# Kernel optimization log

Hardware: AMD Instinct MI355X
Metric: run time of the kernel (lower is better)

The kernel has to match this reference:

```python
import jax, jax.numpy as jnp
import numpy as np

INTER = 128  # in_channels // reduction

def conv1x1(x, w, b):
    # x: [B, Cin, H, W], w: [Cout, Cin], b: [Cout]
    return jnp.einsum('bchw,oc->bohw', x, w) + b[None, :, None, None]

def setup_inputs() -> dict:
    key = jax.random.key(0)
    ks = jax.random.split(key, 10)
    B, Cq, Cr, H, W = 4, 256, 512, 64, 64
    std = 0.01
    return {
        'query':     jax.random.normal(ks[0], (B, Cq, H, W), jnp.float32),
        'reference': jax.random.normal(ks[1], (B, Cr, H, W), jnp.float32),
        'Wg': jax.random.normal(ks[2], (INTER, Cr), jnp.float32) * std,
        'bg': jnp.zeros((INTER,), jnp.float32),
        'Wt': jax.random.normal(ks[3], (INTER, Cq), jnp.float32) * std,
        'bt': jnp.zeros((INTER,), jnp.float32),
        'Wp': jax.random.normal(ks[4], (INTER, Cr), jnp.float32) * std,
        'bp': jnp.zeros((INTER,), jnp.float32),
        'Wo': jax.random.normal(ks[5], (Cq, INTER), jnp.float32) * std,
        'bo': jnp.zeros((Cq,), jnp.float32),
    }

def reference(query, reference, Wg, bg, Wt, bt, Wp, bp, Wo, bo):
    B, Cq, H, W = query.shape
    HWq = H * W
    _, Cr, Hr, Wr = reference.shape
    HWr = Hr * Wr
    # 1x1-conv projections
    g_x     = conv1x1(reference, Wg, bg).reshape(B, INTER, HWr).transpose(0, 2, 1)  # [B, HWr, C']
    theta_x = conv1x1(query,     Wt, bt).reshape(B, INTER, HWq).transpose(0, 2, 1)  # [B, HWq, C']
    phi_x   = conv1x1(reference, Wp, bp).reshape(B, INTER, HWr)                     # [B, C', HWr]
    # embedded_gaussian with use_scale: scale by 1/sqrt(inter_channels)
    scores = jnp.einsum('bqc,bck->bqk', theta_x, phi_x) / jnp.sqrt(jnp.float32(INTER))
    pw = jax.nn.softmax(scores, axis=-1)                                            # [B, HWq, HWr]
    y = jnp.einsum('bqk,bkc->bqc', pw, g_x)                                          # [B, HWq, C']
    y = y.transpose(0, 2, 1).reshape(B, INTER, H, W)
    return query + conv1x1(y, Wo, bo)
```

## Files before the change

### kernel.cpp

```cpp
#include <hip/hip_runtime.h>
#include <hip/hip_bf16.h>
#include <stdint.h>

typedef short bf16x8 __attribute__((ext_vector_type(8)));
typedef float f32x4  __attribute__((ext_vector_type(4)));
typedef float f32x16 __attribute__((ext_vector_type(16)));
typedef unsigned short u16;
typedef unsigned int   u32;

#define BATCH 4
#define PTOT  4096
#define CINT  128
#define QK_SCALE 0.12751744f

__device__ __forceinline__ u32 pk_bf16(float a, float b) {
  u32 r;
  asm("v_cvt_pk_bf16_f32 %0, %1, %2" : "=v"(r) : "v"(a), "v"(b));
  return r;
}
__device__ __forceinline__ u16 f2bf(float x) { return (u16)pk_bf16(x, x); }
__device__ __forceinline__ float bf2f(u16 v) { return __uint_as_float(((u32)v) << 16); }

__device__ __forceinline__ f32x4 mfma16(bf16x8 a, bf16x8 b, f32x4 c) {
  return __builtin_amdgcn_mfma_f32_16x16x32_bf16(a, b, c, 0, 0, 0);
}
__device__ __forceinline__ f32x16 mfma32(bf16x8 a, bf16x8 b, f32x16 c) {
  return __builtin_amdgcn_mfma_f32_32x32x16_bf16(a, b, c, 0, 0, 0);
}
__device__ __forceinline__ void gload16(const u16* g, u16* l) {
  __builtin_amdgcn_global_load_lds((const __attribute__((address_space(1))) u32*)g,
                                   (__attribute__((address_space(3))) u32*)l, 16, 0, 0);
}
__device__ __forceinline__ bf16x8 mkfrag(float a0, float a1, float a2, float a3,
                                         float a4, float a5, float a6, float a7) {
  u32 A = pk_bf16(a0, a1), B = pk_bf16(a2, a3);
  u32 C = pk_bf16(a4, a5), D = pk_bf16(a6, a7);
  asm volatile("v_permlane32_swap_b32 %0, %1" : "+v"(A), "+v"(C));
  asm volatile("v_permlane32_swap_b32 %0, %1" : "+v"(B), "+v"(D));
  union { u32 w[4]; bf16x8 v; } u;
  u.w[0] = A; u.w[1] = B; u.w[2] = C; u.w[3] = D;
  return u.v;
}

__global__ void k_cvt_all(const float* __restrict__ Wt, const float* __restrict__ Wp,
                          const float* __restrict__ Wg, const float* __restrict__ Wo,
                          u16* __restrict__ dst) {
  int i = (blockIdx.x * 256 + threadIdx.x) * 4;
  const float* s; int off;
  if (i < 32768)       { s = Wt; off = i; }
  else if (i < 98304)  { s = Wp; off = i - 32768; }
  else if (i < 163840) { s = Wg; off = i - 98304; }
  else                 { s = Wo; off = i - 163840; }
  float4 v = *(const float4*)(s + off);
  *(uint2*)(dst + i) = make_uint2(pk_bf16(v.x, v.y), pk_bf16(v.z, v.w));
}

__global__ void k_proj_pix(const float* __restrict__ X, const u16* __restrict__ W,
                           const float* __restrict__ bias, u16* __restrict__ O,
                           int Cin, float scale) {
  const int b = blockIdx.y, p0 = blockIdx.x * 64;
  const int t = threadIdx.x, lane = t & 63, w = t >> 6;
  const int m_ = lane & 15, h = lane >> 4;
  __shared__ __align__(16) u16 At[64][40];
  __shared__ __align__(16) u16 Wl[128][40];
  const float* xb = X + (size_t)b * Cin * PTOT;
  f32x4 acc[4][2];
#pragma unroll
  for (int i = 0; i < 4; i++) { acc[i][0] = (f32x4)0.0f; acc[i][1] = (f32x4)0.0f; }
  const int p = t & 63, cg = t >> 6;
  const int wrow = t >> 1, whalf = t & 1;
  for (int k0 = 0; k0 < Cin; k0 += 32) {
    __syncthreads();
    {
      const float* sx = xb + (size_t)(k0 + 8 * cg) * PTOT + p0 + p;
      float v0 = sx[0],        v1 = sx[PTOT],   v2 = sx[2*PTOT], v3 = sx[3*PTOT];
      float v4 = sx[4*PTOT],   v5 = sx[5*PTOT], v6 = sx[6*PTOT], v7 = sx[7*PTOT];
      *(uint2*)&At[p][8*cg]     = make_uint2(pk_bf16(v0,v1), pk_bf16(v2,v3));
      *(uint2*)&At[p][8*cg + 4] = make_uint2(pk_bf16(v4,v5), pk_bf16(v6,v7));
    }
    {
      const u16* sw = W + (size_t)wrow * Cin + k0 + whalf * 16;
      uint4 a = *(const uint4*)sw, c = *(const uint4*)(sw + 8);
      *(uint4*)&Wl[wrow][whalf*16]     = a;
      *(uint4*)&Wl[wrow][whalf*16 + 8] = c;
    }
    __syncthreads();
    bf16x8 bf0 = *(const bf16x8*)&Wl[w*32 + m_][8*h];
    bf16x8 bf1 = *(const bf16x8*)&Wl[w*32 + 16 + m_][8*h];
#pragma unroll
    for (int mb = 0; mb < 4; mb++) {
      bf16x8 af = *(const bf16x8*)&At[mb*16 + m_][8*h];
      acc[mb][0] = mfma16(af, bf0, acc[mb][0]);
      acc[mb][1] = mfma16(af, bf1, acc[mb][1]);
    }
  }
  u16* ob = O + (size_t)b * PTOT * CINT;
#pragma unroll
  for (int mb = 0; mb < 4; mb++)
#pragma unroll
    for (int nb = 0; nb < 2; nb++) {
      int c = w*32 + nb*16 + m_;
      float bv = bias[c];
#pragma unroll
      for (int r = 0; r < 4; r++) {
        int pp = p0 + mb*16 + 4*h + r;
        ob[(size_t)pp * CINT + c] = f2bf((acc[mb][nb][r] + bv) * scale);
      }
    }
}

__global__ void k_proj_ref(const float* __restrict__ X, const u16* __restrict__ Wp,
                           const u16* __restrict__ Wg, const float* __restrict__ bp,
                           const float* __restrict__ bg, u16* __restrict__ PH,
                           u16* __restrict__ Gm) {
  const int Cin = 512;
  const int b = blockIdx.y, p0 = blockIdx.x * 64;
  const int t = threadIdx.x, lane = t & 63, w = t >> 6;
  const int m_ = lane & 15, h = lane >> 4;
  __shared__ __align__(16) u16 Bt[64][40];
  __shared__ __align__(16) u16 Wpl[128][40];
  __shared__ __align__(16) u16 Wgl[128][40];
  const float* xb = X + (size_t)b * Cin * PTOT;
  f32x4 accp[4][2];
  f32x4 accg[2][4];
#pragma unroll
  for (int i = 0; i < 4; i++) { accp[i][0] = (f32x4)0.0f; accp[i][1] = (f32x4)0.0f; }
#pragma unroll
  for (int i = 0; i < 2; i++)
#pragma unroll
    for (int j = 0; j < 4; j++) accg[i][j] = (f32x4)0.0f;
  const int p = t & 63, cg = t >> 6;
  const int wrow = t >> 1, whalf = t & 1;
  for (int k0 = 0; k0 < Cin; k0 += 32) {
    __syncthreads();
    {
      const float* sx = xb + (size_t)(k0 + 8 * cg) * PTOT + p0 + p;
      float v0 = sx[0],        v1 = sx[PTOT],   v2 = sx[2*PTOT], v3 = sx[3*PTOT];
      float v4 = sx[4*PTOT],   v5 = sx[5*PTOT], v6 = sx[6*PTOT], v7 = sx[7*PTOT];
      *(uint2*)&Bt[p][8*cg]     = make_uint2(pk_bf16(v0,v1), pk_bf16(v2,v3));
      *(uint2*)&Bt[p][8*cg + 4] = make_uint2(pk_bf16(v4,v5), pk_bf16(v6,v7));
    }
    {
      const u16* sw = Wp + (size_t)wrow * Cin + k0 + whalf * 16;
      *(uint4*)&Wpl[wrow][whalf*16]     = *(const uint4*)sw;
      *(uint4*)&Wpl[wrow][whalf*16 + 8] = *(const uint4*)(sw + 8);
      const u16* sg = Wg + (size_t)wrow * Cin + k0 + whalf * 16;
      *(uint4*)&Wgl[wrow][whalf*16]     = *(const uint4*)sg;
      *(uint4*)&Wgl[wrow][whalf*16 + 8] = *(const uint4*)(sg + 8);
    }
    __syncthreads();
    {
      bf16x8 bf0 = *(const bf16x8*)&Wpl[w*32 + m_][8*h];
      bf16x8 bf1 = *(const bf16x8*)&Wpl[w*32 + 16 + m_][8*h];
#pragma unroll
      for (int mb = 0; mb < 4; mb++) {
        bf16x8 af = *(const bf16x8*)&Bt[mb*16 + m_][8*h];
        accp[mb][0] = mfma16(af, bf0, accp[mb][0]);
        accp[mb][1] = mfma16(af, bf1, accp[mb][1]);
      }
    }
    {
      bf16x8 bfr[4];
#pragma unroll
      for (int nb = 0; nb < 4; nb++) bfr[nb] = *(const bf16x8*)&Bt[nb*16 + m_][8*h];
#pragma unroll
      for (int mb = 0; mb < 2; mb++) {
        bf16x8 af = *(const bf16x8*)&Wgl[w*32 + mb*16 + m_][8*h];
#pragma unroll
        for (int nb = 0; nb < 4; nb++) accg[mb][nb] = mfma16(af, bfr[nb], accg[mb][nb]);
      }
    }
  }
  {
    u16* ob = PH + (size_t)b * PTOT * CINT;
#pragma unroll
    for (int mb = 0; mb < 4; mb++)
#pragma unroll
      for (int nb = 0; nb < 2; nb++) {
        int c = w*32 + nb*16 + m_;
        float bv = bp[c];
#pragma unroll
        for (int r = 0; r < 4; r++) {
          int pp = p0 + mb*16 + 4*h + r;
          ob[(size_t)pp * CINT + c] = f2bf(accp[mb][nb][r] + bv);
        }
      }
  }
  {
    u16* ob = Gm + (size_t)b * CINT * PTOT;
#pragma unroll
    for (int mb = 0; mb < 2; mb++)
#pragma unroll
      for (int nb = 0; nb < 4; nb++) {
        int pidx = p0 + nb*16 + m_;
#pragma unroll
        for (int r = 0; r < 4; r++) {
          int c = w*32 + mb*16 + 4*h + r;
          ob[(size_t)c * PTOT + pidx] = f2bf(accg[mb][nb][r] + bg[c]);
        }
      }
  }
}

template<int SPLIT>
__global__ __launch_bounds__(256, 2)
void k_attn(const u16* __restrict__ TH, const u16* __restrict__ PH,
            const u16* __restrict__ G, u16* __restrict__ U,
            float* __restrict__ ML, u16* __restrict__ Y) {
  constexpr int LSPLIT = (SPLIT == 4) ? 2 : ((SPLIT == 2) ? 1 : 0);
  constexpr int NITER = 64 >> LSPLIT;
  const int total = 32 * BATCH * SPLIT;
  const int did = blockIdx.x;
  const int gid = (did & 7) * (total >> 3) + (did >> 3);
  const int qb = gid & 31, grp = gid >> 5;
  const int z = grp & (SPLIT - 1), b = grp >> LSPLIT;
  const int t = threadIdx.x, lane = t & 63, w = t >> 6;
  const int l31 = lane & 31, hi = lane >> 5;
  __shared__ __align__(16) u16 Kl[2][64 * 128];
  __shared__ __align__(16) u16 Vl[2][128 * 64];
  const u16* thb = TH + (size_t)b * PTOT * CINT;
  const u16* phb = PH + (size_t)b * PTOT * CINT;
  const u16* gb  = G  + (size_t)b * CINT * PTOT;
  const int q0 = qb * 128, qw = q0 + w * 32;
  bf16x8 qf[8];
  {
    const u16* qr = thb + (size_t)(qw + l31) * CINT + hi * 8;
#pragma unroll
    for (int cs = 0; cs < 8; cs++) qf[cs] = *(const bf16x8*)(qr + cs * 16);
  }
  f32x16 yacc[4];
#pragma unroll
  for (int i = 0; i < 4; i++) yacc[i] = (f32x16)0.0f;
  float mrun = -3.0e38f, lrun = 0.0f;
  const int it0 = z * NITER;

  auto STAGE = [&](int bb, int it) {
    const int k0 = it * 64;
#pragma unroll
    for (int i = 0; i < 4; i++) {
      const int s = w * 4 + i;
      {
        const int row = s * 4 + (lane >> 4);
        const int x = ((lane & 15) * 8) ^ ((row & 7) << 3);
        gload16(phb + (size_t)(k0 + row) * CINT + x, &Kl[bb][s * 512]);
      }
      {
        const int row = s * 8 + (lane >> 3);
        const int x = ((lane & 7) * 8) ^ ((row & 7) << 3);
        gload16(gb + (size_t)row * PTOT + k0 + x, &Vl[bb][s * 512]);
      }
    }
  };

  int cur = 0;
  STAGE(0, it0);
  for (int it = it0; it < it0 + NITER; ++it) {
    __builtin_amdgcn_s_barrier();
    if (it + 1 < it0 + NITER) {
      STAGE(cur ^ 1, it + 1);
      asm volatile("s_waitcnt vmcnt(8)" ::: "memory");
    } else {
      asm volatile("s_waitcnt vmcnt(0)" ::: "memory");
    }
    __builtin_amdgcn_s_barrier();
    __builtin_amdgcn_sched_barrier(0);
    f32x16 sa0 = (f32x16)0.0f, sa1 = (f32x16)0.0f;
    __builtin_amdgcn_s_setprio(1);
#pragma unroll
    for (int cs = 0; cs < 8; cs++) {
      const int xc = cs * 16 + hi * 8;
      const int r0 = l31, r1 = 32 + l31;
      bf16x8 a0 = *(const bf16x8*)&Kl[cur][r0 * 128 + (xc ^ ((r0 & 7) << 3))];
      bf16x8 a1 = *(const bf16x8*)&Kl[cur][r1 * 128 + (xc ^ ((r1 & 7) << 3))];
      sa0 = mfma32(a0, qf[cs], sa0);
      sa1 = mfma32(a1, qf[cs], sa1);
    }
    __builtin_amdgcn_s_setprio(0);
    float tm = sa0[0];
#pragma unroll
    for (int i = 1; i < 16; i++) tm = fmaxf(tm, sa0[i]);
#pragma unroll
    for (int i = 0; i < 16; i++) tm = fmaxf(tm, sa1[i]);
    tm = fmaxf(tm, __shfl_xor(tm, 32));
    if (!__all(tm <= mrun + 8.0f)) {
      float mnew = fmaxf(mrun, tm);
      float f = exp2f(mrun - mnew);
      mrun = mnew; lrun *= f;
#pragma unroll
      for (int i = 0; i < 4; i++) yacc[i] *= f;
    }
    float e0[16], e1[16], ts = 0.0f;
#pragma unroll
    for (int i = 0; i < 16; i++) { e0[i] = exp2f(sa0[i] - mrun); ts += e0[i]; }
#pragma unroll
    for (int i = 0; i < 16; i++) { e1[i] = exp2f(sa1[i] - mrun); ts += e1[i]; }
    ts += __shfl_xor(ts, 32);
    lrun += ts;
    bf16x8 pa[4];
    pa[0] = mkfrag(e0[0], e0[1], e0[2], e0[3], e0[4], e0[5], e0[6], e0[7]);
    pa[1] = mkfrag(e0[8], e0[9], e0[10], e0[11], e0[12], e0[13], e0[14], e0[15]);
    pa[2] = mkfrag(e1[0], e1[1], e1[2], e1[3], e1[4], e1[5], e1[6], e1[7]);
    pa[3] = mkfrag(e1[8], e1[9], e1[10], e1[11], e1[12], e1[13], e1[14], e1[15]);
    __builtin_amdgcn_s_setprio(1);
#pragma unroll
    for (int fs = 0; fs < 4; fs++) {
      const int xk = fs * 16 + hi * 8;
#pragma unroll
      for (int nt = 0; nt < 4; nt++) {
        const int r = nt * 32 + l31;
        bf16x8 vf = *(const bf16x8*)&Vl[cur][r * 64 + (xk ^ ((r & 7) << 3))];
        yacc[nt] = mfma32(pa[fs], vf, yacc[nt]);
      }
    }
    __builtin_amdgcn_s_setprio(0);
    cur ^= 1;
  }
  if constexpr (SPLIT > 1) {
    u16* ub = U + (size_t)(z * BATCH + b) * PTOT * CINT;
#pragma unroll
    for (int reg = 0; reg < 16; reg++) {
      const int qq = qw + (reg & 3) + 8 * (reg >> 2) + 4 * hi;
      u16* row = ub + (size_t)qq * CINT + l31;
      row[0]  = f2bf(yacc[0][reg]);
      row[32] = f2bf(yacc[1][reg]);
      row[64] = f2bf(yacc[2][reg]);
      row[96] = f2bf(yacc[3][reg]);
    }
    if (lane < 32) {
      float* mlb = ML + ((size_t)(z * BATCH + b) * PTOT + qw + lane) * 2;
      mlb[0] = mrun; mlb[1] = lrun;
    }
  } else {
    const float inv = 1.0f / lrun;
    u16* yb = Y + (size_t)b * PTOT * CINT;
#pragma unroll
    for (int reg = 0; reg < 16; reg++) {
      const int qq = qw + (reg & 3) + 8 * (reg >> 2) + 4 * hi;
      u16* row = yb + (size_t)qq * CINT + l31;
      row[0]  = f2bf(yacc[0][reg] * inv);
      row[32] = f2bf(yacc[1][reg] * inv);
      row[64] = f2bf(yacc[2][reg] * inv);
      row[96] = f2bf(yacc[3][reg] * inv);
    }
  }
}

template<int SPLIT>
__global__ void k_combine(const u16* __restrict__ U, const float* __restrict__ ML,
                          u16* __restrict__ Y) {
  int tid = blockIdx.x * 256 + threadIdx.x;
  int c8 = (tid & 15) * 8;
  int q  = (tid >> 4) & (PTOT - 1);
  int b  = tid >> 16;
  float ms[SPLIT], ls[SPLIT];
  float M = -3.0e38f;
#pragma unroll
  for (int s = 0; s < SPLIT; s++) {
    const float* p = ML + ((size_t)(s * BATCH + b) * PTOT + q) * 2;
    ms[s] = p[0]; ls[s] = p[1];
    M = fmaxf(M, ms[s]);
  }
  float L = 0.0f;
#pragma unroll
  for (int s = 0; s < SPLIT; s++) { ms[s] = exp2f(ms[s] - M); L += ls[s] * ms[s]; }
  float inv = 1.0f / L;
  float acc[8];
#pragma unroll
  for (int j = 0; j < 8; j++) acc[j] = 0.0f;
#pragma unroll
  for (int s = 0; s < SPLIT; s++) {
    const u16* up = U + ((size_t)(s * BATCH + b) * PTOT + q) * CINT + c8;
    uint4 v = *(const uint4*)up;
    float f = ms[s];
    acc[0] += bf2f((u16)(v.x & 0xffff)) * f;  acc[1] += bf2f((u16)(v.x >> 16)) * f;
    acc[2] += bf2f((u16)(v.y & 0xffff)) * f;  acc[3] += bf2f((u16)(v.y >> 16)) * f;
    acc[4] += bf2f((u16)(v.z & 0xffff)) * f;  acc[5] += bf2f((u16)(v.z >> 16)) * f;
    acc[6] += bf2f((u16)(v.w & 0xffff)) * f;  acc[7] += bf2f((u16)(v.w >> 16)) * f;
  }
  uint4 o;
  o.x = pk_bf16(acc[0] * inv, acc[1] * inv);
  o.y = pk_bf16(acc[2] * inv, acc[3] * inv);
  o.z = pk_bf16(acc[4] * inv, acc[5] * inv);
  o.w = pk_bf16(acc[6] * inv, acc[7] * inv);
  *(uint4*)(Y + ((size_t)b * PTOT + q) * CINT + c8) = o;
}

__global__ void k_outproj(const float* __restrict__ Q, const u16* __restrict__ Wo,
                          const float* __restrict__ bo, const u16* __restrict__ Y,
                          float* __restrict__ O) {
  const int p0 = blockIdx.x * 64, chh = blockIdx.y, b = blockIdx.z;
  const int t = threadIdx.x, lane = t & 63, w = t >> 6;
  const int m_ = lane & 15, h = lane >> 4;
  __shared__ __align__(16) u16 Wl[128][136];
  __shared__ __align__(16) u16 Yl[64][136];
  {
    int row = t >> 1, cc = t & 1;
    const u16* src = Wo + (size_t)(chh*128 + row) * CINT + cc*64;
#pragma unroll
    for (int i = 0; i < 8; i++)
      *(uint4*)&Wl[row][cc*64 + i*8] = *(const uint4*)(src + i*8);
  }
  {
    int row = t >> 2, cc = t & 3;
    const u16* src = Y + ((size_t)b * PTOT + p0 + row) * CINT + cc*32;
#pragma unroll
    for (int i = 0; i < 4; i++)
      *(uint4*)&Yl[row][cc*32 + i*8] = *(const uint4*)(src + i*8);
  }
  __syncthreads();
  f32x4 acc[2][4];
#pragma unroll
  for (int i = 0; i < 2; i++)
#pragma unroll
    for (int j = 0; j < 4; j++) acc[i][j] = (f32x4)0.0f;
#pragma unroll
  for (int ks = 0; ks < 4; ks++) {
    bf16x8 bfr[4];
#pragma unroll
    for (int nb = 0; nb < 4; nb++) bfr[nb] = *(const bf16x8*)&Yl[nb*16 + m_][ks*32 + 8*h];
#pragma unroll
    for (int mb = 0; mb < 2; mb++) {
      bf16x8 af = *(const bf16x8*)&Wl[w*32 + mb*16 + m_][ks*32 + 8*h];
#pragma unroll
      for (int nb = 0; nb < 4; nb++) acc[mb][nb] = mfma16(af, bfr[nb], acc[mb][nb]);
    }
  }
  const size_t cob = (size_t)b * 256 + (size_t)chh * 128;
#pragma unroll
  for (int mb = 0; mb < 2; mb++)
#pragma unroll
    for (int nb = 0; nb < 4; nb++) {
      int pidx = p0 + nb*16 + m_;
#pragma unroll
      for (int r = 0; r < 4; r++) {
        int co = w*32 + mb*16 + 4*h + r;
        size_t idx = (cob + co) * PTOT + pidx;
        O[idx] = Q[idx] + acc[mb][nb][r] + bo[chh*128 + co];
      }
    }
}

extern "C" void kernel_launch(void* const* d_in, const int* in_sizes, int n_in,
                              void* d_out, int out_size, void* d_ws, size_t ws_size,
                              hipStream_t stream) {
  const float* q_in = (const float*)d_in[0];
  const float* ref  = (const float*)d_in[1];
  const float* Wg   = (const float*)d_in[2];
  const float* bg   = (const float*)d_in[3];
  const float* Wt   = (const float*)d_in[4];
  const float* bt   = (const float*)d_in[5];
  const float* Wp   = (const float*)d_in[6];
  const float* bp   = (const float*)d_in[7];
  const float* Wo   = (const float*)d_in[8];
  const float* bo   = (const float*)d_in[9];
  float* out = (float*)d_out;
  char* ws = (char*)d_ws;

  u16* WB  = (u16*)ws;
  u16* WtB = WB;
  u16* WpB = WB + 32768;
  u16* WgB = WB + 98304;
  u16* WoB = WB + 163840;
  u16* TH  = (u16*)(ws + 393216);
  u16* PH  = (u16*)(ws + 4587520);
  u16* G   = (u16*)(ws + 8781824);
  u16* U   = (u16*)(ws + 12976128);
  const size_t NEED4 = 12976128 + 16777216 + 524288;
  const size_t NEED2 = 12976128 +  8388608 + 262144;
  int split = (ws_size >= NEED4) ? 4 : (ws_size >= NEED2) ? 2 : 1;
  float* ML = (float*)(ws + 12976128 + (size_t)split * 4194304);
  u16* Y = (split > 1) ? TH : (u16*)(ws + 12976128);

  k_cvt_all<<<192, 256, 0, stream>>>(Wt, Wp, Wg, Wo, WB);

  dim3 gp(64, BATCH);
  k_proj_pix<<<gp, 256, 0, stream>>>(q_in, WtB, bt, TH, 256, QK_SCALE);
  k_proj_ref<<<gp, 256, 0, stream>>>(ref, WpB, WgB, bp, bg, PH, G);

  if (split == 4) {
    k_attn<4><<<512, 256, 0, stream>>>(TH, PH, G, U, ML, Y);
    k_combine<4><<<1024, 256, 0, stream>>>(U, ML, Y);
  } else if (split == 2) {
    k_attn<2><<<256, 256, 0, stream>>>(TH, PH, G, U, ML, Y);
    k_combine<2><<<1024, 256, 0, stream>>>(U, ML, Y);
  } else {
    k_attn<1><<<128, 256, 0, stream>>>(TH, PH, G, U, ML, Y);
  }

  dim3 go(64, 2, BATCH);
  k_outproj<<<go, 256, 0, stream>>>(q_in, WoB, bo, Y, out);
}
```

Baseline: 193.7 us.

## Fuse projections, weight conversion and split combine; rework attention pipeline

```diff
diff --git a/kernel.cpp b/kernel.cpp
--- a/kernel.cpp
+++ b/kernel.cpp
@@ -20,6 +20,9 @@
 }
 __device__ __forceinline__ u16 f2bf(float x) { return (u16)pk_bf16(x, x); }
 __device__ __forceinline__ float bf2f(u16 v) { return __uint_as_float(((u32)v) << 16); }
+__device__ __forceinline__ float max3f(float a, float b, float c) {
+  return fmaxf(fmaxf(a, b), c);
+}
 
 __device__ __forceinline__ f32x4 mfma16(bf16x8 a, bf16x8 b, f32x4 c) {
   return __builtin_amdgcn_mfma_f32_16x16x32_bf16(a, b, c, 0, 0, 0);
@@ -42,168 +45,159 @@
   return u.v;
 }
 
-__global__ void k_cvt_all(const float* __restrict__ Wt, const float* __restrict__ Wp,
-                          const float* __restrict__ Wg, const float* __restrict__ Wo,
-                          u16* __restrict__ dst) {
-  int i = (blockIdx.x * 256 + threadIdx.x) * 4;
-  const float* s; int off;
-  if (i < 32768)       { s = Wt; off = i; }
-  else if (i < 98304)  { s = Wp; off = i - 32768; }
-  else if (i < 163840) { s = Wg; off = i - 98304; }
-  else                 { s = Wo; off = i - 163840; }
-  float4 v = *(const float4*)(s + off);
-  *(uint2*)(dst + i) = make_uint2(pk_bf16(v.x, v.y), pk_bf16(v.z, v.w));
-}
-
-__global__ void k_proj_pix(const float* __restrict__ X, const u16* __restrict__ W,
-                           const float* __restrict__ bias, u16* __restrict__ O,
-                           int Cin, float scale) {
-  const int b = blockIdx.y, p0 = blockIdx.x * 64;
-  const int t = threadIdx.x, lane = t & 63, w = t >> 6;
-  const int m_ = lane & 15, h = lane >> 4;
-  __shared__ __align__(16) u16 At[64][40];
-  __shared__ __align__(16) u16 Wl[128][40];
-  const float* xb = X + (size_t)b * Cin * PTOT;
-  f32x4 acc[4][2];
-#pragma unroll
-  for (int i = 0; i < 4; i++) { acc[i][0] = (f32x4)0.0f; acc[i][1] = (f32x4)0.0f; }
-  const int p = t & 63, cg = t >> 6;
-  const int wrow = t >> 1, whalf = t & 1;
-  for (int k0 = 0; k0 < Cin; k0 += 32) {
-    __syncthreads();
-    {
-      const float* sx = xb + (size_t)(k0 + 8 * cg) * PTOT + p0 + p;
-      float v0 = sx[0],        v1 = sx[PTOT],   v2 = sx[2*PTOT], v3 = sx[3*PTOT];
-      float v4 = sx[4*PTOT],   v5 = sx[5*PTOT], v6 = sx[6*PTOT], v7 = sx[7*PTOT];
-      *(uint2*)&At[p][8*cg]     = make_uint2(pk_bf16(v0,v1), pk_bf16(v2,v3));
-      *(uint2*)&At[p][8*cg + 4] = make_uint2(pk_bf16(v4,v5), pk_bf16(v6,v7));
-    }
-    {
-      const u16* sw = W + (size_t)wrow * Cin + k0 + whalf * 16;
-      uint4 a = *(const uint4*)sw, c = *(const uint4*)(sw + 8);
-      *(uint4*)&Wl[wrow][whalf*16]     = a;
-      *(uint4*)&Wl[wrow][whalf*16 + 8] = c;
-    }
-    __syncthreads();
-    bf16x8 bf0 = *(const bf16x8*)&Wl[w*32 + m_][8*h];
-    bf16x8 bf1 = *(const bf16x8*)&Wl[w*32 + 16 + m_][8*h];
-#pragma unroll
-    for (int mb = 0; mb < 4; mb++) {
-      bf16x8 af = *(const bf16x8*)&At[mb*16 + m_][8*h];
-      acc[mb][0] = mfma16(af, bf0, acc[mb][0]);
-      acc[mb][1] = mfma16(af, bf1, acc[mb][1]);
-    }
-  }
-  u16* ob = O + (size_t)b * PTOT * CINT;
-#pragma unroll
-  for (int mb = 0; mb < 4; mb++)
-#pragma unroll
-    for (int nb = 0; nb < 2; nb++) {
-      int c = w*32 + nb*16 + m_;
-      float bv = bias[c];
-#pragma unroll
-      for (int r = 0; r < 4; r++) {
-        int pp = p0 + mb*16 + 4*h + r;
-        ob[(size_t)pp * CINT + c] = f2bf((acc[mb][nb][r] + bv) * scale);
-      }
-    }
-}
-
-__global__ void k_proj_ref(const float* __restrict__ X, const u16* __restrict__ Wp,
-                           const u16* __restrict__ Wg, const float* __restrict__ bp,
-                           const float* __restrict__ bg, u16* __restrict__ PH,
-                           u16* __restrict__ Gm) {
-  const int Cin = 512;
+__global__ void k_proj_all(const float* __restrict__ Xq, const float* __restrict__ Xr,
+                           const float* __restrict__ Wt, const float* __restrict__ bt,
+                           const float* __restrict__ Wp, const float* __restrict__ bp,
+                           const float* __restrict__ Wg, const float* __restrict__ bg,
+                           u16* __restrict__ TH, u16* __restrict__ PH, u16* __restrict__ Gm) {
   const int b = blockIdx.y, p0 = blockIdx.x * 64;
   const int t = threadIdx.x, lane = t & 63, w = t >> 6;
   const int m_ = lane & 15, h = lane >> 4;
   __shared__ __align__(16) u16 Bt[64][40];
-  __shared__ __align__(16) u16 Wpl[128][40];
-  __shared__ __align__(16) u16 Wgl[128][40];
-  const float* xb = X + (size_t)b * Cin * PTOT;
-  f32x4 accp[4][2];
-  f32x4 accg[2][4];
-#pragma unroll
-  for (int i = 0; i < 4; i++) { accp[i][0] = (f32x4)0.0f; accp[i][1] = (f32x4)0.0f; }
-#pragma unroll
-  for (int i = 0; i < 2; i++)
-#pragma unroll
-    for (int j = 0; j < 4; j++) accg[i][j] = (f32x4)0.0f;
+  __shared__ __align__(16) u16 W1[128][40];
+  __shared__ __align__(16) u16 W2[128][40];
   const int p = t & 63, cg = t >> 6;
   const int wrow = t >> 1, whalf = t & 1;
-  for (int k0 = 0; k0 < Cin; k0 += 32) {
-    __syncthreads();
-    {
-      const float* sx = xb + (size_t)(k0 + 8 * cg) * PTOT + p0 + p;
-      float v0 = sx[0],        v1 = sx[PTOT],   v2 = sx[2*PTOT], v3 = sx[3*PTOT];
-      float v4 = sx[4*PTOT],   v5 = sx[5*PTOT], v6 = sx[6*PTOT], v7 = sx[7*PTOT];
-      *(uint2*)&Bt[p][8*cg]     = make_uint2(pk_bf16(v0,v1), pk_bf16(v2,v3));
-      *(uint2*)&Bt[p][8*cg + 4] = make_uint2(pk_bf16(v4,v5), pk_bf16(v6,v7));
-    }
-    {
-      const u16* sw = Wp + (size_t)wrow * Cin + k0 + whalf * 16;
-      *(uint4*)&Wpl[wrow][whalf*16]     = *(const uint4*)sw;
-      *(uint4*)&Wpl[wrow][whalf*16 + 8] = *(const uint4*)(sw + 8);
-      const u16* sg = Wg + (size_t)wrow * Cin + k0 + whalf * 16;
-      *(uint4*)&Wgl[wrow][whalf*16]     = *(const uint4*)sg;
-      *(uint4*)&Wgl[wrow][whalf*16 + 8] = *(const uint4*)(sg + 8);
-    }
-    __syncthreads();
-    {
-      bf16x8 bf0 = *(const bf16x8*)&Wpl[w*32 + m_][8*h];
-      bf16x8 bf1 = *(const bf16x8*)&Wpl[w*32 + 16 + m_][8*h];
+  if (blockIdx.z == 0) {
+    const int Cin = 256;
+    const float* xb = Xq + (size_t)b * Cin * PTOT;
+    f32x4 acc[4][2];
+#pragma unroll
+    for (int i = 0; i < 4; i++) { acc[i][0] = (f32x4)0.0f; acc[i][1] = (f32x4)0.0f; }
+    for (int k0 = 0; k0 < Cin; k0 += 32) {
+      __syncthreads();
+      {
+        const float* sx = xb + (size_t)(k0 + 8 * cg) * PTOT + p0 + p;
+        float v0 = sx[0],        v1 = sx[PTOT],   v2 = sx[2*PTOT], v3 = sx[3*PTOT];
+        float v4 = sx[4*PTOT],   v5 = sx[5*PTOT], v6 = sx[6*PTOT], v7 = sx[7*PTOT];
+        *(uint2*)&Bt[p][8*cg]     = make_uint2(pk_bf16(v0,v1), pk_bf16(v2,v3));
+        *(uint2*)&Bt[p][8*cg + 4] = make_uint2(pk_bf16(v4,v5), pk_bf16(v6,v7));
+      }
+      {
+        const float* sw = Wt + (size_t)wrow * Cin + k0 + whalf * 16;
+        float4 w0 = *(const float4*)sw,     w1 = *(const float4*)(sw + 4);
+        float4 w2 = *(const float4*)(sw+8), w3 = *(const float4*)(sw + 12);
+        *(uint4*)&W1[wrow][whalf*16]   = make_uint4(pk_bf16(w0.x,w0.y), pk_bf16(w0.z,w0.w),
+                                                    pk_bf16(w1.x,w1.y), pk_bf16(w1.z,w1.w));
+        *(uint4*)&W1[wrow][whalf*16+8] = make_uint4(pk_bf16(w2.x,w2.y), pk_bf16(w2.z,w2.w),
+                                                    pk_bf16(w3.x,w3.y), pk_bf16(w3.z,w3.w));
+      }
+      __syncthreads();
+      bf16x8 bf0 = *(const bf16x8*)&W1[w*32 + m_][8*h];
+      bf16x8 bf1 = *(const bf16x8*)&W1[w*32 + 16 + m_][8*h];
 #pragma unroll
       for (int mb = 0; mb < 4; mb++) {
         bf16x8 af = *(const bf16x8*)&Bt[mb*16 + m_][8*h];
-        accp[mb][0] = mfma16(af, bf0, accp[mb][0]);
-        accp[mb][1] = mfma16(af, bf1, accp[mb][1]);
-      }
-    }
-    {
-      bf16x8 bfr[4];
-#pragma unroll
-      for (int nb = 0; nb < 4; nb++) bfr[nb] = *(const bf16x8*)&Bt[nb*16 + m_][8*h];
-#pragma unroll
-      for (int mb = 0; mb < 2; mb++) {
-        bf16x8 af = *(const bf16x8*)&Wgl[w*32 + mb*16 + m_][8*h];
-#pragma unroll
-        for (int nb = 0; nb < 4; nb++) accg[mb][nb] = mfma16(af, bfr[nb], accg[mb][nb]);
-      }
-    }
-  }
-  {
-    u16* ob = PH + (size_t)b * PTOT * CINT;
+        acc[mb][0] = mfma16(af, bf0, acc[mb][0]);
+        acc[mb][1] = mfma16(af, bf1, acc[mb][1]);
+      }
+    }
+    u16* ob = TH + (size_t)b * PTOT * CINT;
 #pragma unroll
     for (int mb = 0; mb < 4; mb++)
 #pragma unroll
       for (int nb = 0; nb < 2; nb++) {
         int c = w*32 + nb*16 + m_;
-        float bv = bp[c];
+        float bv = bt[c];
 #pragma unroll
         for (int r = 0; r < 4; r++) {
           int pp = p0 + mb*16 + 4*h + r;
-          ob[(size_t)pp * CINT + c] = f2bf(accp[mb][nb][r] + bv);
+          ob[(size_t)pp * CINT + c] = f2bf((acc[mb][nb][r] + bv) * QK_SCALE);
         }
       }
-  }
-  {
-    u16* ob = Gm + (size_t)b * CINT * PTOT;
-#pragma unroll
-    for (int mb = 0; mb < 2; mb++)
-#pragma unroll
-      for (int nb = 0; nb < 4; nb++) {
-        int pidx = p0 + nb*16 + m_;
-#pragma unroll
-        for (int r = 0; r < 4; r++) {
-          int c = w*32 + mb*16 + 4*h + r;
-          ob[(size_t)c * PTOT + pidx] = f2bf(accg[mb][nb][r] + bg[c]);
+  } else {
+    const int Cin = 512;
+    const float* xb = Xr + (size_t)b * Cin * PTOT;
+    f32x4 accp[4][2];
+    f32x4 accg[2][4];
+#pragma unroll
+    for (int i = 0; i < 4; i++) { accp[i][0] = (f32x4)0.0f; accp[i][1] = (f32x4)0.0f; }
+#pragma unroll
+    for (int i = 0; i < 2; i++)
+#pragma unroll
+      for (int j = 0; j < 4; j++) accg[i][j] = (f32x4)0.0f;
+    for (int k0 = 0; k0 < Cin; k0 += 32) {
+      __syncthreads();
+      {
+        const float* sx = xb + (size_t)(k0 + 8 * cg) * PTOT + p0 + p;
+        float v0 = sx[0],        v1 = sx[PTOT],   v2 = sx[2*PTOT], v3 = sx[3*PTOT];
+        float v4 = sx[4*PTOT],   v5 = sx[5*PTOT], v6 = sx[6*PTOT], v7 = sx[7*PTOT];
+        *(uint2*)&Bt[p][8*cg]     = make_uint2(pk_bf16(v0,v1), pk_bf16(v2,v3));
+        *(uint2*)&Bt[p][8*cg + 4] = make_uint2(pk_bf16(v4,v5), pk_bf16(v6,v7));
+      }
+      {
+        const float* sw = Wp + (size_t)wrow * Cin + k0 + whalf * 16;
+        float4 w0 = *(const float4*)sw,     w1 = *(const float4*)(sw + 4);
+        float4 w2 = *(const float4*)(sw+8), w3 = *(const float4*)(sw + 12);
+        *(uint4*)&W1[wrow][whalf*16]   = make_uint4(pk_bf16(w0.x,w0.y), pk_bf16(w0.z,w0.w),
+                                                    pk_bf16(w1.x,w1.y), pk_bf16(w1.z,w1.w));
+        *(uint4*)&W1[wrow][whalf*16+8] = make_uint4(pk_bf16(w2.x,w2.y), pk_bf16(w2.z,w2.w),
+                                                    pk_bf16(w3.x,w3.y), pk_bf16(w3.z,w3.w));
+        const float* sg = Wg + (size_t)wrow * Cin + k0 + whalf * 16;
+        float4 g0 = *(const float4*)sg,     g1 = *(const float4*)(sg + 4);
+        float4 g2 = *(const float4*)(sg+8), g3 = *(const float4*)(sg + 12);
+        *(uint4*)&W2[wrow][whalf*16]   = make_uint4(pk_bf16(g0.x,g0.y), pk_bf16(g0.z,g0.w),
+                                                    pk_bf16(g1.x,g1.y), pk_bf16(g1.z,g1.w));
+        *(uint4*)&W2[wrow][whalf*16+8] = make_uint4(pk_bf16(g2.x,g2.y), pk_bf16(g2.z,g2.w),
+                                                    pk_bf16(g3.x,g3.y), pk_bf16(g3.z,g3.w));
+      }
+      __syncthreads();
+      {
+        bf16x8 bf0 = *(const bf16x8*)&W1[w*32 + m_][8*h];
+        bf16x8 bf1 = *(const bf16x8*)&W1[w*32 + 16 + m_][8*h];
+#pragma unroll
+        for (int mb = 0; mb < 4; mb++) {
+          bf16x8 af = *(const bf16x8*)&Bt[mb*16 + m_][8*h];
+          accp[mb][0] = mfma16(af, bf0, accp[mb][0]);
+          accp[mb][1] = mfma16(af, bf1, accp[mb][1]);
         }
       }
+      {
+        bf16x8 bfr[4];
+#pragma unroll
+        for (int nb = 0; nb < 4; nb++) bfr[nb] = *(const bf16x8*)&Bt[nb*16 + m_][8*h];
+#pragma unroll
+        for (int mb = 0; mb < 2; mb++) {
+          bf16x8 af = *(const bf16x8*)&W2[w*32 + mb*16 + m_][8*h];
+#pragma unroll
+          for (int nb = 0; nb < 4; nb++) accg[mb][nb] = mfma16(af, bfr[nb], accg[mb][nb]);
+        }
+      }
+    }
+    {
+      u16* ob = PH + (size_t)b * PTOT * CINT;
+#pragma unroll
+      for (int mb = 0; mb < 4; mb++)
+#pragma unroll
+        for (int nb = 0; nb < 2; nb++) {
+          int c = w*32 + nb*16 + m_;
+          float bv = bp[c];
+#pragma unroll
+          for (int r = 0; r < 4; r++) {
+            int pp = p0 + mb*16 + 4*h + r;
+            ob[(size_t)pp * CINT + c] = f2bf(accp[mb][nb][r] + bv);
+          }
+        }
+    }
+    {
+      u16* ob = Gm + (size_t)b * CINT * PTOT;
+#pragma unroll
+      for (int mb = 0; mb < 2; mb++)
+#pragma unroll
+        for (int nb = 0; nb < 4; nb++) {
+          int pidx = p0 + nb*16 + m_;
+#pragma unroll
+          for (int r = 0; r < 4; r++) {
+            int c = w*32 + mb*16 + 4*h + r;
+            ob[(size_t)c * PTOT + pidx] = f2bf(accg[mb][nb][r] + bg[c]);
+          }
+        }
+    }
   }
 }
 
 template<int SPLIT>
-__global__ __launch_bounds__(256, 2)
+__global__ __launch_bounds__(256, 3)
 void k_attn(const u16* __restrict__ TH, const u16* __restrict__ PH,
             const u16* __restrict__ G, u16* __restrict__ U,
             float* __restrict__ ML, u16* __restrict__ Y) {
@@ -217,90 +211,124 @@
   const int t = threadIdx.x, lane = t & 63, w = t >> 6;
   const int l31 = lane & 31, hi = lane >> 5;
   __shared__ __align__(16) u16 Kl[2][64 * 128];
-  __shared__ __align__(16) u16 Vl[2][128 * 64];
+  __shared__ __align__(16) u16 Vl[128 * 64];
+  __shared__ float Ls[4][32];
   const u16* thb = TH + (size_t)b * PTOT * CINT;
   const u16* phb = PH + (size_t)b * PTOT * CINT;
   const u16* gb  = G  + (size_t)b * CINT * PTOT;
-  const int q0 = qb * 128, qw = q0 + w * 32;
+  const int qw = qb * 128 + w * 32;
   bf16x8 qf[8];
   {
     const u16* qr = thb + (size_t)(qw + l31) * CINT + hi * 8;
 #pragma unroll
     for (int cs = 0; cs < 8; cs++) qf[cs] = *(const bf16x8*)(qr + cs * 16);
   }
+  bf16x8 ones;
+  {
+    union { u32 w[4]; bf16x8 v; } u;
+    u.w[0] = u.w[1] = u.w[2] = u.w[3] = 0x3F803F80u;
+    ones = u.v;
+  }
   f32x16 yacc[4];
 #pragma unroll
   for (int i = 0; i < 4; i++) yacc[i] = (f32x16)0.0f;
-  float mrun = -3.0e38f, lrun = 0.0f;
+  f32x16 lacc = (f32x16)0.0f;
+  float mrun = -3.0e38f;
   const int it0 = z * NITER;
 
-  auto STAGE = [&](int bb, int it) {
+  auto STAGE_K = [&](int bb, int it) {
     const int k0 = it * 64;
 #pragma unroll
     for (int i = 0; i < 4; i++) {
       const int s = w * 4 + i;
-      {
-        const int row = s * 4 + (lane >> 4);
-        const int x = ((lane & 15) * 8) ^ ((row & 7) << 3);
-        gload16(phb + (size_t)(k0 + row) * CINT + x, &Kl[bb][s * 512]);
-      }
-      {
-        const int row = s * 8 + (lane >> 3);
-        const int x = ((lane & 7) * 8) ^ ((row & 7) << 3);
-        gload16(gb + (size_t)row * PTOT + k0 + x, &Vl[bb][s * 512]);
-      }
+      const int row = s * 4 + (lane >> 4);
+      const int cl = ((lane & 15) * 8) ^ ((row & 15) << 3);
+      gload16(phb + (size_t)(k0 + row) * CINT + cl, &Kl[bb][s * 512]);
     }
   };
-
+  auto STAGE_V = [&](int it) {
+    const int k0 = it * 64;
+#pragma unroll
+    for (int i = 0; i < 4; i++) {
+      const int s = w * 4 + i;
+      const int row = s * 8 + (lane >> 3);
+      const int cl = ((lane & 7) * 8) ^ ((row & 7) << 3);
+      gload16(gb + (size_t)row * PTOT + k0 + cl, &Vl[s * 512]);
+    }
+  };
+
+  STAGE_K(0, it0);
   int cur = 0;
-  STAGE(0, it0);
   for (int it = it0; it < it0 + NITER; ++it) {
-    __builtin_amdgcn_s_barrier();
-    if (it + 1 < it0 + NITER) {
-      STAGE(cur ^ 1, it + 1);
-      asm volatile("s_waitcnt vmcnt(8)" ::: "memory");
-    } else {
-      asm volatile("s_waitcnt vmcnt(0)" ::: "memory");
-    }
+    asm volatile("s_waitcnt vmcnt(0)" ::: "memory");
     __builtin_amdgcn_s_barrier();
     __builtin_amdgcn_sched_barrier(0);
+    STAGE_V(it);
+    const int itn = (it + 1 < it0 + NITER) ? it + 1 : it;
+    STAGE_K(cur ^ 1, itn);
     f32x16 sa0 = (f32x16)0.0f, sa1 = (f32x16)0.0f;
     __builtin_amdgcn_s_setprio(1);
 #pragma unroll
     for (int cs = 0; cs < 8; cs++) {
       const int xc = cs * 16 + hi * 8;
       const int r0 = l31, r1 = 32 + l31;
-      bf16x8 a0 = *(const bf16x8*)&Kl[cur][r0 * 128 + (xc ^ ((r0 & 7) << 3))];
-      bf16x8 a1 = *(const bf16x8*)&Kl[cur][r1 * 128 + (xc ^ ((r1 & 7) << 3))];
+      bf16x8 a0 = *(const bf16x8*)&Kl[cur][r0 * 128 + (xc ^ ((r0 & 15) << 3))];
+      bf16x8 a1 = *(const bf16x8*)&Kl[cur][r1 * 128 + (xc ^ ((r1 & 15) << 3))];
       sa0 = mfma32(a0, qf[cs], sa0);
       sa1 = mfma32(a1, qf[cs], sa1);
     }
     __builtin_amdgcn_s_setprio(0);
-    float tm = sa0[0];
-#pragma unroll
-    for (int i = 1; i < 16; i++) tm = fmaxf(tm, sa0[i]);
-#pragma unroll
-    for (int i = 0; i < 16; i++) tm = fmaxf(tm, sa1[i]);
-    tm = fmaxf(tm, __shfl_xor(tm, 32));
+    float t0 = max3f(sa0[0],  sa0[1],  sa0[2]);
+    float t1 = max3f(sa0[3],  sa0[4],  sa0[5]);
+    float t2 = max3f(sa0[6],  sa0[7],  sa0[8]);
+    float t3 = max3f(sa0[9],  sa0[10], sa0[11]);
+    float t4 = max3f(sa0[12], sa0[13], sa0[14]);
+    float t5 = max3f(sa1[0],  sa1[1],  sa1[2]);
+    float t6 = max3f(sa1[3],  sa1[4],  sa1[5]);
+    float t7 = max3f(sa1[6],  sa1[7],  sa1[8]);
+    float t8 = max3f(sa1[9],  sa1[10], sa1[11]);
+    float t9 = max3f(sa1[12], sa1[13], sa1[14]);
+    float ta = fmaxf(sa0[15], sa1[15]);
+    float u0 = max3f(t0, t1, t2);
+    float u1 = max3f(t3, t4, t5);
+    float u2 = max3f(t6, t7, t8);
+    float u3 = max3f(t9, ta, u0);
+    float tm = max3f(u1, u2, u3);
+    {
+      u32 xa = __float_as_uint(tm), xb = xa;
+      asm volatile("v_permlane32_swap_b32 %0, %1" : "+v"(xa), "+v"(xb));
+      tm = fmaxf(tm, fmaxf(__uint_as_float(xa), __uint_as_float(xb)));
+    }
     if (!__all(tm <= mrun + 8.0f)) {
       float mnew = fmaxf(mrun, tm);
       float f = exp2f(mrun - mnew);
-      mrun = mnew; lrun *= f;
+      mrun = mnew;
+      lacc *= f;
 #pragma unroll
       for (int i = 0; i < 4; i++) yacc[i] *= f;
     }
-    float e0[16], e1[16], ts = 0.0f;
-#pragma unroll
-    for (int i = 0; i < 16; i++) { e0[i] = exp2f(sa0[i] - mrun); ts += e0[i]; }
-#pragma unroll
-    for (int i = 0; i < 16; i++) { e1[i] = exp2f(sa1[i] - mrun); ts += e1[i]; }
-    ts += __shfl_xor(ts, 32);
-    lrun += ts;
     bf16x8 pa[4];
-    pa[0] = mkfrag(e0[0], e0[1], e0[2], e0[3], e0[4], e0[5], e0[6], e0[7]);
-    pa[1] = mkfrag(e0[8], e0[9], e0[10], e0[11], e0[12], e0[13], e0[14], e0[15]);
-    pa[2] = mkfrag(e1[0], e1[1], e1[2], e1[3], e1[4], e1[5], e1[6], e1[7]);
-    pa[3] = mkfrag(e1[8], e1[9], e1[10], e1[11], e1[12], e1[13], e1[14], e1[15]);
+    pa[0] = mkfrag(exp2f(sa0[0] - mrun),  exp2f(sa0[1] - mrun),  exp2f(sa0[2] - mrun),
+                   exp2f(sa0[3] - mrun),  exp2f(sa0[4] - mrun),  exp2f(sa0[5] - mrun),
+                   exp2f(sa0[6] - mrun),  exp2f(sa0[7] - mrun));
+    pa[1] = mkfrag(exp2f(sa0[8] - mrun),  exp2f(sa0[9] - mrun),  exp2f(sa0[10] - mrun),
+                   exp2f(sa0[11] - mrun), exp2f(sa0[12] - mrun), exp2f(sa0[13] - mrun),
+                   exp2f(sa0[14] - mrun), exp2f(sa0[15] - mrun));
+    pa[2] = mkfrag(exp2f(sa1[0] - mrun),  exp2f(sa1[1] - mrun),  exp2f(sa1[2] - mrun),
+                   exp2f(sa1[3] - mrun),  exp2f(sa1[4] - mrun),  exp2f(sa1[5] - mrun),
+                   exp2f(sa1[6] - mrun),  exp2f(sa1[7] - mrun));
+    pa[3] = mkfrag(exp2f(sa1[8] - mrun),  exp2f(sa1[9] - mrun),  exp2f(sa1[10] - mrun),
+                   exp2f(sa1[11] - mrun), exp2f(sa1[12] - mrun), exp2f(sa1[13] - mrun),
+                   exp2f(sa1[14] - mrun), exp2f(sa1[15] - mrun));
+    __builtin_amdgcn_s_setprio(1);
+    lacc = mfma32(pa[0], ones, lacc);
+    lacc = mfma32(pa[1], ones, lacc);
+    lacc = mfma32(pa[2], ones, lacc);
+    lacc = mfma32(pa[3], ones, lacc);
+    __builtin_amdgcn_s_setprio(0);
+    asm volatile("s_waitcnt vmcnt(4)" ::: "memory");
+    __builtin_amdgcn_s_barrier();
+    __builtin_amdgcn_sched_barrier(0);
     __builtin_amdgcn_s_setprio(1);
 #pragma unroll
     for (int fs = 0; fs < 4; fs++) {
@@ -308,7 +336,7 @@
 #pragma unroll
       for (int nt = 0; nt < 4; nt++) {
         const int r = nt * 32 + l31;
-        bf16x8 vf = *(const bf16x8*)&Vl[cur][r * 64 + (xk ^ ((r & 7) << 3))];
+        bf16x8 vf = *(const bf16x8*)&Vl[r * 64 + (xk ^ ((r & 7) << 3))];
         yacc[nt] = mfma32(pa[fs], vf, yacc[nt]);
       }
     }
@@ -326,12 +354,24 @@
       row[64] = f2bf(yacc[2][reg]);
       row[96] = f2bf(yacc[3][reg]);
     }
-    if (lane < 32) {
-      float* mlb = ML + ((size_t)(z * BATCH + b) * PTOT + qw + lane) * 2;
-      mlb[0] = mrun; mlb[1] = lrun;
-    }
+    float* mlb = ML + (size_t)(z * BATCH + b) * PTOT * 2;
+    if (l31 == 0) {
+#pragma unroll
+      for (int reg = 0; reg < 16; reg++) {
+        const int row = (reg & 3) + 8 * (reg >> 2) + 4 * hi;
+        mlb[(size_t)(qw + row) * 2 + 1] = lacc[reg];
+      }
+    }
+    if (lane < 32) mlb[(size_t)(qw + lane) * 2] = mrun;
   } else {
-    const float inv = 1.0f / lrun;
+    if (l31 == 0) {
+#pragma unroll
+      for (int reg = 0; reg < 16; reg++)
+        Ls[w][(reg & 3) + 8 * (reg >> 2) + 4 * hi] = lacc[reg];
+    }
+    asm volatile("s_waitcnt lgkmcnt(0)" ::: "memory");
+    __builtin_amdgcn_sched_barrier(0);
+    const float inv = 1.0f / Ls[w][l31];
     u16* yb = Y + (size_t)b * PTOT * CINT;
 #pragma unroll
     for (int reg = 0; reg < 16; reg++) {
@@ -346,48 +386,9 @@
 }
 
 template<int SPLIT>
-__global__ void k_combine(const u16* __restrict__ U, const float* __restrict__ ML,
-                          u16* __restrict__ Y) {
-  int tid = blockIdx.x * 256 + threadIdx.x;
-  int c8 = (tid & 15) * 8;
-  int q  = (tid >> 4) & (PTOT - 1);
-  int b  = tid >> 16;
-  float ms[SPLIT], ls[SPLIT];
-  float M = -3.0e38f;
-#pragma unroll
-  for (int s = 0; s < SPLIT; s++) {
-    const float* p = ML + ((size_t)(s * BATCH + b) * PTOT + q) * 2;
-    ms[s] = p[0]; ls[s] = p[1];
-    M = fmaxf(M, ms[s]);
-  }
-  float L = 0.0f;
-#pragma unroll
-  for (int s = 0; s < SPLIT; s++) { ms[s] = exp2f(ms[s] - M); L += ls[s] * ms[s]; }
-  float inv = 1.0f / L;
-  float acc[8];
-#pragma unroll
-  for (int j = 0; j < 8; j++) acc[j] = 0.0f;
-#pragma unroll
-  for (int s = 0; s < SPLIT; s++) {
-    const u16* up = U + ((size_t)(s * BATCH + b) * PTOT + q) * CINT + c8;
-    uint4 v = *(const uint4*)up;
-    float f = ms[s];
-    acc[0] += bf2f((u16)(v.x & 0xffff)) * f;  acc[1] += bf2f((u16)(v.x >> 16)) * f;
-    acc[2] += bf2f((u16)(v.y & 0xffff)) * f;  acc[3] += bf2f((u16)(v.y >> 16)) * f;
-    acc[4] += bf2f((u16)(v.z & 0xffff)) * f;  acc[5] += bf2f((u16)(v.z >> 16)) * f;
-    acc[6] += bf2f((u16)(v.w & 0xffff)) * f;  acc[7] += bf2f((u16)(v.w >> 16)) * f;
-  }
-  uint4 o;
-  o.x = pk_bf16(acc[0] * inv, acc[1] * inv);
-  o.y = pk_bf16(acc[2] * inv, acc[3] * inv);
-  o.z = pk_bf16(acc[4] * inv, acc[5] * inv);
-  o.w = pk_bf16(acc[6] * inv, acc[7] * inv);
-  *(uint4*)(Y + ((size_t)b * PTOT + q) * CINT + c8) = o;
-}
-
-__global__ void k_outproj(const float* __restrict__ Q, const u16* __restrict__ Wo,
-                          const float* __restrict__ bo, const u16* __restrict__ Y,
-                          float* __restrict__ O) {
+__global__ void k_outproj(const float* __restrict__ Q, const float* __restrict__ Wo,
+                          const float* __restrict__ bo, const u16* __restrict__ UY,
+                          const float* __restrict__ ML, float* __restrict__ O) {
   const int p0 = blockIdx.x * 64, chh = blockIdx.y, b = blockIdx.z;
   const int t = threadIdx.x, lane = t & 63, w = t >> 6;
   const int m_ = lane & 15, h = lane >> 4;
@@ -395,17 +396,53 @@
   __shared__ __align__(16) u16 Yl[64][136];
   {
     int row = t >> 1, cc = t & 1;
-    const u16* src = Wo + (size_t)(chh*128 + row) * CINT + cc*64;
-#pragma unroll
-    for (int i = 0; i < 8; i++)
-      *(uint4*)&Wl[row][cc*64 + i*8] = *(const uint4*)(src + i*8);
+    const float* src = Wo + (size_t)(chh*128 + row) * CINT + cc*64;
+#pragma unroll
+    for (int i = 0; i < 8; i++) {
+      float4 a = *(const float4*)(src + i*8), c = *(const float4*)(src + i*8 + 4);
+      *(uint4*)&Wl[row][cc*64 + i*8] = make_uint4(pk_bf16(a.x,a.y), pk_bf16(a.z,a.w),
+                                                  pk_bf16(c.x,c.y), pk_bf16(c.z,c.w));
+    }
   }
   {
     int row = t >> 2, cc = t & 3;
-    const u16* src = Y + ((size_t)b * PTOT + p0 + row) * CINT + cc*32;
-#pragma unroll
-    for (int i = 0; i < 4; i++)
-      *(uint4*)&Yl[row][cc*32 + i*8] = *(const uint4*)(src + i*8);
+    int p = p0 + row;
+    if constexpr (SPLIT > 1) {
+      float msv[SPLIT], lsv[SPLIT];
+      float M = -3.0e38f;
+#pragma unroll
+      for (int s = 0; s < SPLIT; s++) {
+        const float* mp = ML + ((size_t)(s * BATCH + b) * PTOT + p) * 2;
+        msv[s] = mp[0]; lsv[s] = mp[1];
+        M = fmaxf(M, msv[s]);
+      }
+      float L = 0.0f;
+#pragma unroll
+      for (int s = 0; s < SPLIT; s++) { msv[s] = exp2f(msv[s] - M); L += lsv[s] * msv[s]; }
+      float inv = 1.0f / L;
+#pragma unroll
+      for (int s = 0; s < SPLIT; s++) msv[s] *= inv;
+#pragma unroll
+      for (int i = 0; i < 4; i++) {
+        float a0 = 0, a1 = 0, a2 = 0, a3 = 0, a4 = 0, a5 = 0, a6 = 0, a7 = 0;
+#pragma unroll
+        for (int s = 0; s < SPLIT; s++) {
+          uint4 v = *(const uint4*)(UY + ((size_t)(s * BATCH + b) * PTOT + p) * CINT + cc*32 + i*8);
+          float f = msv[s];
+          a0 += bf2f((u16)(v.x & 0xffff)) * f;  a1 += bf2f((u16)(v.x >> 16)) * f;
+          a2 += bf2f((u16)(v.y & 0xffff)) * f;  a3 += bf2f((u16)(v.y >> 16)) * f;
+          a4 += bf2f((u16)(v.z & 0xffff)) * f;  a5 += bf2f((u16)(v.z >> 16)) * f;
+          a6 += bf2f((u16)(v.w & 0xffff)) * f;  a7 += bf2f((u16)(v.w >> 16)) * f;
+        }
+        *(uint4*)&Yl[row][cc*32 + i*8] = make_uint4(pk_bf16(a0,a1), pk_bf16(a2,a3),
+                                                    pk_bf16(a4,a5), pk_bf16(a6,a7));
+      }
+    } else {
+      const u16* src = UY + ((size_t)b * PTOT + p) * CINT + cc*32;
+#pragma unroll
+      for (int i = 0; i < 4; i++)
+        *(uint4*)&Yl[row][cc*32 + i*8] = *(const uint4*)(src + i*8);
+    }
   }
   __syncthreads();
   f32x4 acc[2][4];
@@ -456,37 +493,27 @@
   float* out = (float*)d_out;
   char* ws = (char*)d_ws;
 
-  u16* WB  = (u16*)ws;
-  u16* WtB = WB;
-  u16* WpB = WB + 32768;
-  u16* WgB = WB + 98304;
-  u16* WoB = WB + 163840;
-  u16* TH  = (u16*)(ws + 393216);
-  u16* PH  = (u16*)(ws + 4587520);
-  u16* G   = (u16*)(ws + 8781824);
-  u16* U   = (u16*)(ws + 12976128);
-  const size_t NEED4 = 12976128 + 16777216 + 524288;
-  const size_t NEED2 = 12976128 +  8388608 + 262144;
+  u16* TH = (u16*)(ws + 0);
+  u16* PH = (u16*)(ws + 4194304);
+  u16* G  = (u16*)(ws + 8388608);
+  u16* U  = (u16*)(ws + 12582912);
+  const size_t NEED4 = 12582912 + 4u*4194304 + 524288;
+  const size_t NEED2 = 12582912 + 2u*4194304 + 262144;
   int split = (ws_size >= NEED4) ? 4 : (ws_size >= NEED2) ? 2 : 1;
-  float* ML = (float*)(ws + 12976128 + (size_t)split * 4194304);
-  u16* Y = (split > 1) ? TH : (u16*)(ws + 12976128);
-
-  k_cvt_all<<<192, 256, 0, stream>>>(Wt, Wp, Wg, Wo, WB);
-
-  dim3 gp(64, BATCH);
-  k_proj_pix<<<gp, 256, 0, stream>>>(q_in, WtB, bt, TH, 256, QK_SCALE);
-  k_proj_ref<<<gp, 256, 0, stream>>>(ref, WpB, WgB, bp, bg, PH, G);
-
+  float* ML = (float*)(ws + 12582912 + (size_t)split * 4194304);
+
+  dim3 gp(64, BATCH, 2);
+  k_proj_all<<<gp, 256, 0, stream>>>(q_in, ref, Wt, bt, Wp, bp, Wg, bg, TH, PH, G);
+
+  dim3 go(64, 2, BATCH);
   if (split == 4) {
-    k_attn<4><<<512, 256, 0, stream>>>(TH, PH, G, U, ML, Y);
-    k_combine<4><<<1024, 256, 0, stream>>>(U, ML, Y);
+    k_attn<4><<<512, 256, 0, stream>>>(TH, PH, G, U, ML, U);
+    k_outproj<4><<<go, 256, 0, stream>>>(q_in, Wo, bo, U, ML, out);
   } else if (split == 2) {
-    k_attn<2><<<256, 256, 0, stream>>>(TH, PH, G, U, ML, Y);
-    k_combine<2><<<1024, 256, 0, stream>>>(U, ML, Y);
+    k_attn<2><<<256, 256, 0, stream>>>(TH, PH, G, U, ML, U);
+    k_outproj<2><<<go, 256, 0, stream>>>(q_in, Wo, bo, U, ML, out);
   } else {
-    k_attn<1><<<128, 256, 0, stream>>>(TH, PH, G, U, ML, Y);
-  }
-
-  dim3 go(64, 2, BATCH);
-  k_outproj<<<go, 256, 0, stream>>>(q_in, WoB, bo, Y, out);
-}
+    k_attn<1><<<128, 256, 0, stream>>>(TH, PH, G, U, ML, U);
+    k_outproj<1><<<go, 256, 0, stream>>>(q_in, Wo, bo, U, ML, out);
+  }
+}
```

New measurement: 243.8 us. 25.9% more time.
